# Performance work log

Hardware: AMD Instinct MI355X
Metric: run time of the kernel (lower is better)

Reference implementation:

```python
import jax, jax.numpy as jnp
import numpy as np

N_NODES = 100000
N_EDGES = 1600000
IN_F = 256
OUT_F = 128


def setup_inputs() -> dict:
    key = jax.random.key(0)
    k1, k2, k3, k4, k5, k6 = jax.random.split(key, 6)
    x = jax.random.normal(k1, (N_NODES, IN_F), dtype=jnp.float32)
    edge_row = jax.random.randint(k2, (N_EDGES,), 0, N_NODES, dtype=jnp.int32)
    edge_col = jax.random.randint(k3, (N_EDGES,), 0, N_NODES, dtype=jnp.int32)
    edge_val = jax.random.uniform(k4, (N_EDGES,), dtype=jnp.float32)
    # xavier_uniform for W: bound = sqrt(6/(fan_in+fan_out))
    bound_w = float(np.sqrt(6.0 / (IN_F + OUT_F)))
    W = jax.random.uniform(k5, (IN_F, OUT_F), dtype=jnp.float32, minval=-bound_w, maxval=bound_w)
    stdv = 1.0 / float(np.sqrt(OUT_F))
    b = jax.random.uniform(k6, (OUT_F,), dtype=jnp.float32, minval=-stdv, maxval=stdv)
    return {"x": x, "edge_row": edge_row, "edge_col": edge_col, "edge_val": edge_val, "W": W, "b": b}


def reference(x, edge_row, edge_col, edge_val, W, b):
    # dropout p=0.0 -> identity
    support = x @ W + b                      # [N, out]
    # sparse adjacency matmul: out[r] += val * support[c] over edges (r, c, val)
    msgs = edge_val[:, None] * support[edge_col]          # [E, out]
    out = jax.ops.segment_sum(msgs, edge_row, num_segments=N_NODES)  # [N, out]
    return jax.nn.relu(out)
```

## Files before the change

### kernel.cpp

```cpp
#include <hip/hip_runtime.h>


constexpr int kNodes = 100000;
constexpr int kEdges = 1600000;
constexpr int kInF   = 256;
constexpr int kOutF  = 128;
constexpr int kTiles = kNodes / 16;
constexpr int kBucketBlocks = 800;
constexpr int kGemmBlocks = 1250;

constexpr int kNB = 256;
constexpr int kRB = 391;
constexpr int kCap = 7424;

typedef __attribute__((ext_vector_type(8))) short short8;
typedef __attribute__((ext_vector_type(8))) unsigned short ush8;
typedef __attribute__((ext_vector_type(4))) float floatx4;

__device__ inline unsigned short f2bf_rne(float f) {
    unsigned int u = __float_as_uint(f);
    unsigned int r = u + 0x7FFFu + ((u >> 16) & 1u);
    return (unsigned short)(r >> 16);
}
__device__ inline float bf2f(unsigned short h) {
    return __uint_as_float(((unsigned int)h) << 16);
}

__device__ inline short8 cvt8_bf16(const float4 a, const float4 b) {
    union { short8 s; unsigned int u[4]; } r;
    asm("v_cvt_pk_bf16_f32 %0, %1, %2" : "=v"(r.u[0]) : "v"(a.x), "v"(a.y));
    asm("v_cvt_pk_bf16_f32 %0, %1, %2" : "=v"(r.u[1]) : "v"(a.z), "v"(a.w));
    asm("v_cvt_pk_bf16_f32 %0, %1, %2" : "=v"(r.u[2]) : "v"(b.x), "v"(b.y));
    asm("v_cvt_pk_bf16_f32 %0, %1, %2" : "=v"(r.u[3]) : "v"(b.z), "v"(b.w));
    return r.s;
}

__device__ inline void gload_lds16(const void* g, void* l) {
    __builtin_amdgcn_global_load_lds(
        (const __attribute__((address_space(1))) unsigned int*)g,
        (__attribute__((address_space(3))) unsigned int*)l,
        16, 0, 0);
}

__global__ __launch_bounds__(256) void gcn_gemm(const float* __restrict__ x,
                                                const float* __restrict__ W,
                                                const float* __restrict__ b,
                                                unsigned short* __restrict__ support) {
    __shared__ __align__(16) float lbuf[2][4096];

    const int lane = threadIdx.x & 63;
    const int wv   = threadIdx.x >> 6;
    const int rowl = lane & 15;
    const int quad = lane >> 4;
    const int colbase = wv * 32;

    short8 bfrag[2][8];
#pragma unroll
    for (int ct = 0; ct < 2; ++ct) {
        const int col = colbase + ct * 16 + rowl;
#pragma unroll
        for (int kc = 0; kc < 8; ++kc) {
            const int kb = kc * 32 + quad * 8;
            short8 f;
#pragma unroll
            for (int j = 0; j < 8; ++j)
                f[j] = (short)f2bf_rne(W[(size_t)(kb + j) * kOutF + col]);
            bfrag[ct][kc] = f;
        }
    }
    const float bias0 = b[colbase + rowl];
    const float bias1 = b[colbase + 16 + rowl];

    const int G = gridDim.x;
    int t = blockIdx.x;

#define GEMM_STAGE(buf_, tile_)                                                   \
    do {                                                                          \
        const float* tb_ = x + (size_t)(tile_) * 16 * kInF;                       \
        _Pragma("unroll")                                                         \
        for (int i_ = 0; i_ < 4; ++i_) {                                          \
            const int row_ = i_ * 4 + wv;                                         \
            gload_lds16(tb_ + (size_t)row_ * kInF + ((lane ^ (row_ & 7)) << 2),   \
                        &lbuf[buf_][row_ << 8]);                                  \
        }                                                                         \
    } while (0)

    if (t < kTiles) GEMM_STAGE(0, t);
    int cur = 0;

    for (; t < kTiles; t += G) {
        const int tn = t + G;
        asm volatile("s_waitcnt vmcnt(0)" ::: "memory");
        __syncthreads();
        if (tn < kTiles) GEMM_STAGE(cur ^ 1, tn);

        const int r0 = t * 16;
        const float* base = &lbuf[cur][rowl << 8];
        const int rsw = rowl & 7;
        floatx4 acc0 = {0.f, 0.f, 0.f, 0.f};
        floatx4 acc1 = {0.f, 0.f, 0.f, 0.f};
#pragma unroll
        for (int kc = 0; kc < 8; ++kc) {
            const int g0 = (kc << 3) + (quad << 1);
            const float4 v0 = *reinterpret_cast<const float4*>(base + ((g0 ^ rsw) << 2));
            const float4 v1 = *reinterpret_cast<const float4*>(base + (((g0 + 1) ^ rsw) << 2));
            const short8 a = cvt8_bf16(v0, v1);
            acc0 = __builtin_amdgcn_mfma_f32_16x16x32_bf16(a, bfrag[0][kc], acc0, 0, 0, 0);
            acc1 = __builtin_amdgcn_mfma_f32_16x16x32_bf16(a, bfrag[1][kc], acc1, 0, 0, 0);
        }
#pragma unroll
        for (int reg = 0; reg < 4; ++reg) {
            const size_t rbase = (size_t)(r0 + quad * 4 + reg) * kOutF + colbase;
            support[rbase + rowl]      = f2bf_rne(acc0[reg] + bias0);
            support[rbase + 16 + rowl] = f2bf_rne(acc1[reg] + bias1);
        }
        cur ^= 1;
    }
#undef GEMM_STAGE
}

__global__ __launch_bounds__(256) void gcn_bhist(const int* __restrict__ erow,
                                                 int* __restrict__ bucket_tot) {
    __shared__ int cnt[kNB];
    cnt[threadIdx.x] = 0;
    __syncthreads();
    const int stride = gridDim.x * blockDim.x;
    for (int e = blockIdx.x * blockDim.x + threadIdx.x; e < kEdges; e += stride)
        atomicAdd(&cnt[(unsigned int)erow[e] / (unsigned int)kRB], 1);
    __syncthreads();
    const int c = cnt[threadIdx.x];
    if (c) atomicAdd(&bucket_tot[threadIdx.x], c);
}

__global__ __launch_bounds__(256) void gcn_bscan(const int* __restrict__ bucket_tot,
                                                 int* __restrict__ bucket_base,
                                                 int* __restrict__ bucket_cursor,
                                                 int* __restrict__ row_start) {
    __shared__ int s[256];
    const int v = bucket_tot[threadIdx.x];
    s[threadIdx.x] = v;
    __syncthreads();
#pragma unroll
    for (int off = 1; off < 256; off <<= 1) {
        const int t = (threadIdx.x >= off) ? s[threadIdx.x - off] : 0;
        __syncthreads();
        s[threadIdx.x] += t;
        __syncthreads();
    }
    const int excl = s[threadIdx.x] - v;
    bucket_base[threadIdx.x]   = excl;
    bucket_cursor[threadIdx.x] = excl;
    if (threadIdx.x == 255) {
        bucket_base[256]   = kEdges;
        row_start[kNodes]  = kEdges;
    }
}

__global__ __launch_bounds__(256) void gcn_bin(const int* __restrict__ erow,
                                               const int* __restrict__ ecol,
                                               const float* __restrict__ eval,
                                               int* __restrict__ bucket_cursor,
                                               int2* __restrict__ packed) {
    __shared__ int cnt[kNB];
    __shared__ int base[kNB];
    __shared__ int rk[kNB];
    const int T   = kBucketBlocks * 256;
    const int tid = blockIdx.x * 256 + threadIdx.x;

    cnt[threadIdx.x] = 0;
    rk[threadIdx.x]  = 0;

    int bk[8], pk[8], vb[8];
    bool ok[8];
#pragma unroll
    for (int i = 0; i < 8; ++i) {
        const int e = tid + i * T;
        ok[i] = (e < kEdges);
        const int r = ok[i] ? erow[e] : 0;
        const int c = ok[i] ? ecol[e] : 0;
        const float v = ok[i] ? eval[e] : 0.f;
        const unsigned int b = (unsigned int)r / (unsigned int)kRB;
        bk[i] = (int)b;
        pk[i] = ((r - (int)b * kRB) << 17) | c;
        vb[i] = __float_as_int(v);
    }
    __syncthreads();
#pragma unroll
    for (int i = 0; i < 8; ++i)
        if (ok[i]) atomicAdd(&cnt[bk[i]], 1);
    __syncthreads();
    const int c = cnt[threadIdx.x];
    base[threadIdx.x] = c ? atomicAdd(&bucket_cursor[threadIdx.x], c) : 0;
    __syncthreads();
#pragma unroll
    for (int i = 0; i < 8; ++i) {
        if (ok[i]) {
            const int r = atomicAdd(&rk[bk[i]], 1);
            packed[base[bk[i]] + r] = make_int2(pk[i], vb[i]);
        }
    }
}

__global__ __launch_bounds__(256) void gcn_place(const int* __restrict__ bucket_base,
                                                 int* __restrict__ row_start,
                                                 int2* __restrict__ packed) {
    __shared__ int2 st[kCap];
    __shared__ int  s[512];
    __shared__ int  rcur[kRB + 1];
    const int bk = blockIdx.x;
    const int r0 = bk * kRB;
    const int r1 = min(r0 + kRB, kNodes);
    const int NR = r1 - r0;
    if (NR <= 0) return;
    const int bb = bucket_base[bk];
    const int s1 = bucket_base[bk + 1];
    const int size   = s1 - bb;
    const int staged = min(size, kCap);
    const int tid = threadIdx.x;

    s[tid] = 0;
    s[tid + 256] = 0;
    __syncthreads();

    for (int i = tid; i < staged; i += 256) {
        const int2 p = packed[bb + i];
        st[i] = p;
        atomicAdd(&s[p.x >> 17], 1);
    }
    int2 tail[8];
    int  nt = 0;
    for (int i = kCap + tid; i < size; i += 256) {
        if (nt < 8) {
            tail[nt] = packed[bb + i];
            atomicAdd(&s[tail[nt].x >> 17], 1);
            ++nt;
        }
    }
    __syncthreads();

    const int i0 = tid, i1 = tid + 256;
#pragma unroll
    for (int off = 1; off < 512; off <<= 1) {
        const int v0 = (i0 >= off) ? s[i0 - off] : 0;
        const int v1 = (i1 >= off) ? s[i1 - off] : 0;
        __syncthreads();
        s[i0] += v0;
        s[i1] += v1;
        __syncthreads();
    }

    for (int i = tid; i < NR; i += 256) {
        const int excl = i ? s[i - 1] : 0;
        row_start[r0 + i] = bb + excl;
        rcur[i] = excl;
    }
    __syncthreads();

    for (int i = tid; i < staged; i += 256) {
        const int2 p  = st[i];
        const int pos = bb + atomicAdd(&rcur[p.x >> 17], 1);
        packed[pos] = make_int2(p.x & 0x1FFFF, p.y);
    }
#pragma unroll
    for (int t = 0; t < 8; ++t) {
        if (t < nt) {
            const int2 p  = tail[t];
            const int pos = bb + atomicAdd(&rcur[p.x >> 17], 1);
            packed[pos] = make_int2(p.x & 0x1FFFF, p.y);
        }
    }
}

__global__ __launch_bounds__(256) void gcn_aggregate(const int* __restrict__ row_start,
                                                     const int2* __restrict__ packed,
                                                     const unsigned short* __restrict__ support,
                                                     float* __restrict__ out) {
    const int n  = blockIdx.x * 16 + (threadIdx.x >> 4);
    const int f8 = (threadIdx.x & 15) * 8;
    if (n >= kNodes) return;
    const int s0 = row_start[n];
    const int s1 = row_start[n + 1];
    float acc[8];
#pragma unroll
    for (int j = 0; j < 8; ++j) acc[j] = 0.f;

    int i = s0;
    for (; i + 3 < s1; i += 4) {
        const int2 p0 = packed[i];
        const int2 p1 = packed[i + 1];
        const int2 p2 = packed[i + 2];
        const int2 p3 = packed[i + 3];
        const ush8 a0 = *reinterpret_cast<const ush8*>(support + (size_t)p0.x * kOutF + f8);
        const ush8 a1 = *reinterpret_cast<const ush8*>(support + (size_t)p1.x * kOutF + f8);
        const ush8 a2 = *reinterpret_cast<const ush8*>(support + (size_t)p2.x * kOutF + f8);
        const ush8 a3 = *reinterpret_cast<const ush8*>(support + (size_t)p3.x * kOutF + f8);
        const float v0 = __int_as_float(p0.y), v1 = __int_as_float(p1.y);
        const float v2 = __int_as_float(p2.y), v3 = __int_as_float(p3.y);
#pragma unroll
        for (int j = 0; j < 8; ++j) {
            acc[j] += v0 * bf2f(a0[j]);
            acc[j] += v1 * bf2f(a1[j]);
            acc[j] += v2 * bf2f(a2[j]);
            acc[j] += v3 * bf2f(a3[j]);
        }
    }
    for (; i < s1; ++i) {
        const int2 p = packed[i];
        const float v = __int_as_float(p.y);
        const ush8 a = *reinterpret_cast<const ush8*>(support + (size_t)p.x * kOutF + f8);
#pragma unroll
        for (int j = 0; j < 8; ++j) acc[j] += v * bf2f(a[j]);
    }

    float4 o0 = make_float4(fmaxf(acc[0], 0.f), fmaxf(acc[1], 0.f),
                            fmaxf(acc[2], 0.f), fmaxf(acc[3], 0.f));
    float4 o1 = make_float4(fmaxf(acc[4], 0.f), fmaxf(acc[5], 0.f),
                            fmaxf(acc[6], 0.f), fmaxf(acc[7], 0.f));
    *reinterpret_cast<float4*>(out + (size_t)n * kOutF + f8)     = o0;
    *reinterpret_cast<float4*>(out + (size_t)n * kOutF + f8 + 4) = o1;
}

extern "C" void kernel_launch(void* const* d_in, const int* in_sizes, int n_in,
                              void* d_out, int out_size, void* d_ws, size_t ws_size,
                              hipStream_t stream) {
    const float* x    = (const float*)d_in[0];
    const int*   erow = (const int*)  d_in[1];
    const int*   ecol = (const int*)  d_in[2];
    const float* eval = (const float*)d_in[3];
    const float* W    = (const float*)d_in[4];
    const float* b    = (const float*)d_in[5];
    float* out = (float*)d_out;

    char* ws = (char*)d_ws;
    unsigned short* support = (unsigned short*)(ws);
    int2* packed        = (int2*)(ws + 25600000);
    int*  row_start     = (int*) (ws + 38400000);
    int*  bucket_tot    = (int*) (ws + 38800008);
    int*  bucket_base   = (int*) (ws + 38801032);
    int*  bucket_cursor = (int*) (ws + 38802060);

    gcn_gemm<<<kGemmBlocks, 256, 0, stream>>>(x, W, b, support);

    hipMemsetAsync(bucket_tot, 0, kNB * sizeof(int), stream);
    gcn_bhist<<<1024, 256, 0, stream>>>(erow, bucket_tot);
    gcn_bscan<<<1, 256, 0, stream>>>(bucket_tot, bucket_base, bucket_cursor, row_start);
    gcn_bin  <<<kBucketBlocks, 256, 0, stream>>>(erow, ecol, eval, bucket_cursor, packed);
    gcn_place<<<kNB, 256, 0, stream>>>(bucket_base, row_start, packed);

    gcn_aggregate<<<(kNodes + 15) / 16, 256, 0, stream>>>(row_start, packed, support, out);
}
```

Baseline: 358.5 us.

## Store support in feature-sliced layout and aggregate per 16-column slice

The GEMM now writes the bf16 support matrix as 8 slices of 16 columns, each slice a contiguous [nodes x 16] array. The aggregate kernel is reorganised so that each block handles 64 nodes and one slice, with 4 threads per node each reading 8 bytes. The aim is a smaller gathered working set per block (3.2MB per slice), so slices stay cache-resident across the random column gathers. The cost is 8x more re-reads of the packed edge lists and row_start, narrower 8-byte loads, and scattered 2-byte writes in the GEMM.

```diff
diff --git a/kernel.cpp b/kernel.cpp
--- a/kernel.cpp
+++ b/kernel.cpp
@@ -13,8 +13,11 @@
 constexpr int kRB = 391;
 constexpr int kCap = 7424;
 
+constexpr int kAggTiles = (kNodes + 63) / 64;
+
 typedef __attribute__((ext_vector_type(8))) short short8;
 typedef __attribute__((ext_vector_type(8))) unsigned short ush8;
+typedef __attribute__((ext_vector_type(4))) unsigned short ush4;
 typedef __attribute__((ext_vector_type(4))) float floatx4;
 
 __device__ inline unsigned short f2bf_rne(float f) {
@@ -70,6 +73,9 @@
     }
     const float bias0 = b[colbase + rowl];
     const float bias1 = b[colbase + 16 + rowl];
+
+    unsigned short* s0p = support + (size_t)(wv * 2)     * kNodes * 16 + rowl;
+    unsigned short* s1p = support + (size_t)(wv * 2 + 1) * kNodes * 16 + rowl;
 
     const int G = gridDim.x;
     int t = blockIdx.x;
@@ -110,9 +116,9 @@
         }
 #pragma unroll
         for (int reg = 0; reg < 4; ++reg) {
-            const size_t rbase = (size_t)(r0 + quad * 4 + reg) * kOutF + colbase;
-            support[rbase + rowl]      = f2bf_rne(acc0[reg] + bias0);
-            support[rbase + 16 + rowl] = f2bf_rne(acc1[reg] + bias1);
+            const size_t node = (size_t)(r0 + quad * 4 + reg);
+            s0p[node * 16] = f2bf_rne(acc0[reg] + bias0);
+            s1p[node * 16] = f2bf_rne(acc1[reg] + bias1);
         }
         cur ^= 1;
     }
@@ -275,14 +281,15 @@
                                                      const int2* __restrict__ packed,
                                                      const unsigned short* __restrict__ support,
                                                      float* __restrict__ out) {
-    const int n  = blockIdx.x * 16 + (threadIdx.x >> 4);
-    const int f8 = (threadIdx.x & 15) * 8;
+    const int slice = blockIdx.x & 7;
+    const int tile  = blockIdx.x >> 3;
+    const int n  = tile * 64 + (threadIdx.x >> 2);
+    const int lq = threadIdx.x & 3;
     if (n >= kNodes) return;
+    const unsigned short* sb = support + (size_t)slice * kNodes * 16 + lq * 4;
     const int s0 = row_start[n];
     const int s1 = row_start[n + 1];
-    float acc[8];
-#pragma unroll
-    for (int j = 0; j < 8; ++j) acc[j] = 0.f;
+    float a0 = 0.f, a1 = 0.f, a2 = 0.f, a3 = 0.f;
 
     int i = s0;
     for (; i + 3 < s1; i += 4) {
@@ -290,34 +297,30 @@
         const int2 p1 = packed[i + 1];
         const int2 p2 = packed[i + 2];
         const int2 p3 = packed[i + 3];
-        const ush8 a0 = *reinterpret_cast<const ush8*>(support + (size_t)p0.x * kOutF + f8);
-        const ush8 a1 = *reinterpret_cast<const ush8*>(support + (size_t)p1.x * kOutF + f8);
-        const ush8 a2 = *reinterpret_cast<const ush8*>(support + (size_t)p2.x * kOutF + f8);
-        const ush8 a3 = *reinterpret_cast<const ush8*>(support + (size_t)p3.x * kOutF + f8);
+        const ush4 g0 = *reinterpret_cast<const ush4*>(sb + (size_t)p0.x * 16);
+        const ush4 g1 = *reinterpret_cast<const ush4*>(sb + (size_t)p1.x * 16);
+        const ush4 g2 = *reinterpret_cast<const ush4*>(sb + (size_t)p2.x * 16);
+        const ush4 g3 = *reinterpret_cast<const ush4*>(sb + (size_t)p3.x * 16);
         const float v0 = __int_as_float(p0.y), v1 = __int_as_float(p1.y);
         const float v2 = __int_as_float(p2.y), v3 = __int_as_float(p3.y);
-#pragma unroll
-        for (int j = 0; j < 8; ++j) {
-            acc[j] += v0 * bf2f(a0[j]);
-            acc[j] += v1 * bf2f(a1[j]);
-            acc[j] += v2 * bf2f(a2[j]);
-            acc[j] += v3 * bf2f(a3[j]);
-        }
+        a0 += v0 * bf2f(g0[0]) + v1 * bf2f(g1[0]) + v2 * bf2f(g2[0]) + v3 * bf2f(g3[0]);
+        a1 += v0 * bf2f(g0[1]) + v1 * bf2f(g1[1]) + v2 * bf2f(g2[1]) + v3 * bf2f(g3[1]);
+        a2 += v0 * bf2f(g0[2]) + v1 * bf2f(g1[2]) + v2 * bf2f(g2[2]) + v3 * bf2f(g3[2]);
+        a3 += v0 * bf2f(g0[3]) + v1 * bf2f(g1[3]) + v2 * bf2f(g2[3]) + v3 * bf2f(g3[3]);
     }
     for (; i < s1; ++i) {
         const int2 p = packed[i];
         const float v = __int_as_float(p.y);
-        const ush8 a = *reinterpret_cast<const ush8*>(support + (size_t)p.x * kOutF + f8);
-#pragma unroll
-        for (int j = 0; j < 8; ++j) acc[j] += v * bf2f(a[j]);
-    }
-
-    float4 o0 = make_float4(fmaxf(acc[0], 0.f), fmaxf(acc[1], 0.f),
-                            fmaxf(acc[2], 0.f), fmaxf(acc[3], 0.f));
-    float4 o1 = make_float4(fmaxf(acc[4], 0.f), fmaxf(acc[5], 0.f),
-                            fmaxf(acc[6], 0.f), fmaxf(acc[7], 0.f));
-    *reinterpret_cast<float4*>(out + (size_t)n * kOutF + f8)     = o0;
-    *reinterpret_cast<float4*>(out + (size_t)n * kOutF + f8 + 4) = o1;
+        const ush4 g = *reinterpret_cast<const ush4*>(sb + (size_t)p.x * 16);
+        a0 += v * bf2f(g[0]);
+        a1 += v * bf2f(g[1]);
+        a2 += v * bf2f(g[2]);
+        a3 += v * bf2f(g[3]);
+    }
+
+    const float4 o = make_float4(fmaxf(a0, 0.f), fmaxf(a1, 0.f),
+                                 fmaxf(a2, 0.f), fmaxf(a3, 0.f));
+    *reinterpret_cast<float4*>(out + (size_t)n * kOutF + slice * 16 + lq * 4) = o;
 }
 
 extern "C" void kernel_launch(void* const* d_in, const int* in_sizes, int n_in,
@@ -347,5 +350,5 @@
     gcn_bin  <<<kBucketBlocks, 256, 0, stream>>>(erow, ecol, eval, bucket_cursor, packed);
     gcn_place<<<kNB, 256, 0, stream>>>(bucket_base, row_start, packed);
 
-    gcn_aggregate<<<(kNodes + 15) / 16, 256, 0, stream>>>(row_start, packed, support, out);
-}
+    gcn_aggregate<<<kAggTiles * 8, 256, 0, stream>>>(row_start, packed, support, out);
+}
```

Result: slower. 408.1 us (+13.8%).
